# Performance work log

Measured on AMD Instinct MI355X. Metric: run time of the kernel, lower is better.

Reference implementation:

```python
import jax, jax.numpy as jnp
import numpy as np

N_NODES = 50000
N_EDGES = 800000
N_GRAPHS = 512
IN_DIM, HID_DIM, LAT_DIM = 128, 128, 64


def _glorot(key, fan_in, fan_out):
    lim = np.sqrt(6.0 / (fan_in + fan_out))
    return jax.random.uniform(key, (fan_in, fan_out), jnp.float32, -lim, lim)


def gcn_conv(x, W, b, src, dst, deg_inv_sqrt):
    """PyG GCNConv: out = D^{-1/2}(A+I)D^{-1/2} x W + b (self-loops included)."""
    h = x @ W  # [N, F_out]
    norm = deg_inv_sqrt[src] * deg_inv_sqrt[dst]  # [E]
    msg = h[src] * norm[:, None]  # gather + scale, [E, F_out]
    out = jax.ops.segment_sum(msg, dst, num_segments=x.shape[0])  # scatter-add
    out = out + h * (deg_inv_sqrt * deg_inv_sqrt)[:, None]  # self-loop term
    return out + b


def setup_inputs() -> dict:
    key = jax.random.key(0)
    ks = jax.random.split(key, 12)
    x = jax.random.normal(ks[0], (N_NODES, IN_DIM), jnp.float32)
    edge_index = jax.random.randint(ks[1], (2, N_EDGES), 0, N_NODES, jnp.int64)
    batch = jnp.sort(jax.random.randint(ks[2], (N_NODES,), 0, N_GRAPHS, jnp.int64))
    return {
        "x": x,
        "edge_index": edge_index,
        "batch": batch,
        "W1": _glorot(ks[3], IN_DIM, HID_DIM), "b1": jnp.zeros((HID_DIM,), jnp.float32),
        "W2": _glorot(ks[4], HID_DIM, LAT_DIM), "b2": jnp.zeros((LAT_DIM,), jnp.float32),
        "W3": _glorot(ks[5], LAT_DIM, HID_DIM), "b3": jnp.zeros((HID_DIM,), jnp.float32),
        "W4": _glorot(ks[6], HID_DIM, IN_DIM), "b4": jnp.zeros((IN_DIM,), jnp.float32),
    }


def reference(x, edge_index, batch, W1, b1, W2, b2, W3, b3, W4, b4):
    n = x.shape[0]
    src, dst = edge_index[0], edge_index[1]
    # degrees with self-loops (PyG computes deg over col=dst, +1 for self-loop)
    deg = jax.ops.segment_sum(jnp.ones_like(dst, dtype=x.dtype), dst, num_segments=n) + 1.0
    dis = jax.lax.rsqrt(deg)
    # encoder
    h = jax.nn.relu(gcn_conv(x, W1, b1, src, dst, dis))
    z = gcn_conv(h, W2, b2, src, dst, dis)
    # scatter-mean pooling over graphs
    counts = jax.ops.segment_sum(jnp.ones((n,), x.dtype), batch, num_segments=N_GRAPHS)
    agg = jax.ops.segment_sum(z, batch, num_segments=N_GRAPHS) / jnp.maximum(counts, 1.0)[:, None]
    # decoder
    h2 = jax.nn.relu(gcn_conv(z, W3, b3, src, dst, dis))
    x_hat = gcn_conv(h2, W4, b4, src, dst, dis)
    return (x_hat, z, agg)
```

## Files before the change

kernel.cpp:

```cpp
#include <hip/hip_runtime.h>
#include <hip/hip_fp16.h>
#include <math.h>

#define N_NODES 50000
#define N_EDGES 800000
#define N_GRAPHS 512
#define CAP 62
#define NBINS 196
#define CAPB 5120
#define ABLK 1024
#define PROP_BLOCKS 2048
#define PROP_WAVES (PROP_BLOCKS * 4)

typedef unsigned short u16;
typedef unsigned int u32;
typedef __attribute__((ext_vector_type(8))) short bf16x8_t;
typedef __attribute__((ext_vector_type(4))) float f32x4_t;
typedef __attribute__((ext_vector_type(4))) unsigned int u32x4_t;

constexpr int NBLK_A = (N_EDGES + ABLK - 1) / ABLK;
constexpr int NCW = (49152 + 255) / 256;

__device__ __forceinline__ u16 f2bf(float f) {
    u32 u = __builtin_bit_cast(u32, f);
    return (u16)((u + 0x7fffu + ((u >> 16) & 1u)) >> 16);
}
__device__ __forceinline__ float bf2f(u16 s) {
    return __builtin_bit_cast(float, (u32)s << 16);
}
__device__ __forceinline__ float bf_lo(u32 u) { return __builtin_bit_cast(float, u << 16); }
__device__ __forceinline__ float bf_hi(u32 u) { return __builtin_bit_cast(float, u & 0xffff0000u); }

__device__ __forceinline__ bf16x8_t cvt8(const float* p) {
    float4 a = *reinterpret_cast<const float4*>(p);
    float4 b = *reinterpret_cast<const float4*>(p + 4);
    u32x4_t w;
    w.x = (u32)f2bf(a.x) | ((u32)f2bf(a.y) << 16);
    w.y = (u32)f2bf(a.z) | ((u32)f2bf(a.w) << 16);
    w.z = (u32)f2bf(b.x) | ((u32)f2bf(b.y) << 16);
    w.w = (u32)f2bf(b.z) | ((u32)f2bf(b.w) << 16);
    return __builtin_bit_cast(bf16x8_t, w);
}

__device__ __forceinline__ int block_exscan(int val, int* lds, int tid) {
    lds[tid] = val;
    __syncthreads();
#pragma unroll
    for (int off = 1; off < 256; off <<= 1) {
        int t = (tid >= off) ? lds[tid - off] : 0;
        __syncthreads();
        lds[tid] += t;
        __syncthreads();
    }
    return lds[tid] - val;
}

__global__ __launch_bounds__(256) void pre_scatter(const int* __restrict__ src,
                                                   const int* __restrict__ dst,
                                                   u32* __restrict__ binCnt,
                                                   u32* __restrict__ binList,
                                                   const float* __restrict__ W1, u16* __restrict__ wt1,
                                                   const float* __restrict__ W2, u16* __restrict__ wt2,
                                                   const float* __restrict__ W3, u16* __restrict__ wt3,
                                                   const float* __restrict__ W4, u16* __restrict__ wt4) {
    __shared__ int cur[NBINS];
    __shared__ int lsStart[NBINS];
    __shared__ int gbase[NBINS];
    __shared__ int scanbuf[256];
    __shared__ u32 stage[ABLK];
    __shared__ int gpos[ABLK];
    int t = threadIdx.x;
    if (blockIdx.x >= NBLK_A) {
        int idx = (blockIdx.x - NBLK_A) * 256 + t;
        const float* Wf;
        u16* Wt;
        int K, N, off;
        if (idx < 16384)      { Wf = W1; Wt = wt1; K = 128; N = 128; off = 0; }
        else if (idx < 24576) { Wf = W2; Wt = wt2; K = 128; N = 64;  off = 16384; }
        else if (idx < 32768) { Wf = W3; Wt = wt3; K = 64;  N = 128; off = 24576; }
        else                  { Wf = W4; Wt = wt4; K = 128; N = 128; off = 32768; }
        int q = idx - off;
        int k = q / N, n = q % N;
        Wt[n * K + k] = f2bf(Wf[q]);
        return;
    }
    int e0 = blockIdx.x * ABLK;
    int nEdge = min(ABLK, N_EDGES - e0);

    for (int i = t; i < NBINS; i += 256) cur[i] = 0;
    __syncthreads();

    int myBin[4], myRank[4];
    u32 myPack[4];
    int nmy = 0;
    if (t * 4 < nEdge) {
        nmy = 4;
        int4 dv = *reinterpret_cast<const int4*>(dst + e0 + t * 4);
        int4 sv = *reinterpret_cast<const int4*>(src + e0 + t * 4);
        int ds[4] = {dv.x, dv.y, dv.z, dv.w};
        int ss[4] = {sv.x, sv.y, sv.z, sv.w};
#pragma unroll
        for (int j = 0; j < 4; j++) {
            int d = ds[j];
            int bin = d >> 8;
            myBin[j] = bin;
            myPack[j] = (u32)(ss[j] & 0xFFFF) | ((u32)(d & 0xFF) << 16);
            myRank[j] = atomicAdd(&cur[bin], 1);
        }
    }
    __syncthreads();
    int v = (t < NBINS) ? cur[t] : 0;
    int ex = block_exscan(v, scanbuf, t);
    if (t < NBINS) {
        lsStart[t] = ex;
        gbase[t] = (v > 0) ? (int)atomicAdd(&binCnt[t * 16], (u32)v) : 0;
    }
    __syncthreads();
    for (int j = 0; j < nmy; j++) {
        int bin = myBin[j];
        int idx = lsStart[bin] + myRank[j];
        int p = gbase[bin] + myRank[j];
        stage[idx] = myPack[j];
        gpos[idx] = (p < CAPB) ? (bin * CAPB + p) : -1;
    }
    __syncthreads();
    for (int i = t; i < nEdge; i += 256) {
        int p = gpos[i];
        if (p >= 0) binList[p] = stage[i];
    }
}

__global__ __launch_bounds__(256) void bucket_build(const u32* __restrict__ binList,
                                                    const u32* __restrict__ binCnt,
                                                    u32* __restrict__ bucket,
                                                    float* __restrict__ dis) {
    __shared__ u32 rec[256 * 32];
    int b = blockIdx.x, t = threadIdx.x;
    for (int i = t; i < 256 * 32; i += 256) rec[i] = 0;
    __syncthreads();
    int ecnt = min((int)binCnt[b * 16], CAPB);
    const u32* lst = binList + (size_t)b * CAPB;
    u16* rec16 = reinterpret_cast<u16*>(rec);
    for (int i = t; i < ecnt; i += 256) {
        u32 pk = lst[i];
        int dlow = (pk >> 16) & 0xFF;
        int pos = (int)atomicAdd(&rec[dlow * 32], 1u);
        if (pos < CAP) rec16[dlow * 64 + 2 + pos] = (u16)(pk & 0xFFFF);
    }
    __syncthreads();
    int node0 = b * 256;
    int nNode = min(256, N_NODES - node0);
    for (int i = t; i < nNode * 32; i += 256)
        bucket[(size_t)node0 * 32 + i] = rec[i];
    if (t < nNode) dis[node0 + t] = 1.0f / sqrtf((float)rec[t * 32] + 1.0f);
}

template <int N, int K, bool BIAS, bool RELU, bool SCALE, bool AF32>
__global__ __launch_bounds__(256) void gemm_mfma(const void* __restrict__ Avp,
                                                 const u16* __restrict__ Wt,
                                                 const float* __restrict__ bias,
                                                 const float* __restrict__ dis,
                                                 u16* __restrict__ C) {
    constexpr int KB = K / 32;
    constexpr int TN = N / 64;
    constexpr int TM = (N_NODES + 63) / 64;
    int wave = threadIdx.x >> 6;
    int lane = threadIdx.x & 63;
    int W = blockIdx.x * 4 + wave;
    if (W >= TM * TN) return;
    int tm = W / TN, tn = W % TN;
    int r16 = lane & 15;
    int kg = lane >> 4;

    bf16x8_t bf[4][KB];
#pragma unroll
    for (int nr = 0; nr < 4; nr++) {
        int colg = tn * 64 + nr * 16 + r16;
#pragma unroll
        for (int kb = 0; kb < KB; kb++)
            bf[nr][kb] = *reinterpret_cast<const bf16x8_t*>(Wt + (size_t)colg * K + kb * 32 + kg * 8);
    }

    f32x4_t acc[4][4];
#pragma unroll
    for (int mr = 0; mr < 4; mr++)
#pragma unroll
        for (int nr = 0; nr < 4; nr++)
#pragma unroll
            for (int t = 0; t < 4; t++) acc[mr][nr][t] = 0.f;

#pragma unroll
    for (int mr = 0; mr < 4; mr++) {
        int row = tm * 64 + mr * 16 + r16;
        if (row >= N_NODES) row = N_NODES - 1;
        bf16x8_t af[KB];
#pragma unroll
        for (int kb = 0; kb < KB; kb++) {
            if constexpr (AF32) {
                const float* Af = (const float*)Avp;
                af[kb] = cvt8(Af + (size_t)row * K + kb * 32 + kg * 8);
            } else {
                const u16* Ab = (const u16*)Avp;
                af[kb] = *reinterpret_cast<const bf16x8_t*>(Ab + (size_t)row * K + kb * 32 + kg * 8);
            }
        }
#pragma unroll
        for (int kb = 0; kb < KB; kb++)
#pragma unroll
            for (int nr = 0; nr < 4; nr++)
                acc[mr][nr] = __builtin_amdgcn_mfma_f32_16x16x32_bf16(af[kb], bf[nr][kb],
                                                                      acc[mr][nr], 0, 0, 0);
    }

#pragma unroll
    for (int mr = 0; mr < 4; mr++) {
        float sc[4];
#pragma unroll
        for (int r = 0; r < 4; r++) {
            int row = tm * 64 + mr * 16 + kg * 4 + r;
            sc[r] = (SCALE && row < N_NODES) ? dis[row] : 1.f;
        }
#pragma unroll
        for (int nr = 0; nr < 4; nr++) {
            int colg = tn * 64 + nr * 16 + r16;
            float bv = BIAS ? bias[colg] : 0.f;
#pragma unroll
            for (int r = 0; r < 4; r++) {
                int row = tm * 64 + mr * 16 + kg * 4 + r;
                if (row < N_NODES) {
                    float v = acc[mr][nr][r] + bv;
                    if (RELU) v = fmaxf(v, 0.f);
                    if (SCALE) v *= sc[r];
                    C[(size_t)row * N + colg] = f2bf(v);
                }
            }
        }
    }
}

template <int F, bool RELU, bool BIAS, bool WF32, bool WBF16, bool SCALEOUT>
__global__ __launch_bounds__(256) void propagate_b(const u16* __restrict__ h,
                                                   const u32* __restrict__ bucket,
                                                   const float* __restrict__ dis,
                                                   const float* __restrict__ bias,
                                                   float* __restrict__ out_f,
                                                   u16* __restrict__ out_b) {
    int wid = (blockIdx.x * 256 + threadIdx.x) >> 6;
    int lane = threadIdx.x & 63;
    float2 bv2 = make_float2(0.f, 0.f);
    float bv1 = 0.f;
    if (BIAS) {
        if (F == 128) bv2 = reinterpret_cast<const float2*>(bias)[lane];
        else          bv1 = bias[lane];
    }
    for (int w = wid; w < N_NODES; w += PROP_WAVES) {
        const u32* bw = bucket + (size_t)w * 32;
        int deg = __builtin_amdgcn_readfirstlane(min((int)bw[0], CAP));
        const u16* slots = reinterpret_cast<const u16*>(bw) + 2;
        const u32* sw = reinterpret_cast<const u32*>(reinterpret_cast<const char*>(bw) + 4);
        float di = dis[w];

        if (F == 128) {
            const u32* hw = reinterpret_cast<const u32*>(h);
            float2 a0 = {0.f, 0.f}, a1 = {0.f, 0.f}, a2 = {0.f, 0.f}, a3 = {0.f, 0.f};
            int i = 0;
            for (; i + 16 <= deg; i += 16) {
                u32 cw[8], hv[16];
#pragma unroll
                for (int j = 0; j < 8; j++) cw[j] = sw[(i >> 1) + j];
#pragma unroll
                for (int j = 0; j < 8; j++) {
                    hv[2 * j]     = hw[(size_t)(cw[j] & 0xffffu) * 64 + lane];
                    hv[2 * j + 1] = hw[(size_t)(cw[j] >> 16) * 64 + lane];
                }
#pragma unroll
                for (int j = 0; j < 16; j++) {
                    float lo = bf_lo(hv[j]), hi = bf_hi(hv[j]);
                    if ((j & 3) == 0) { a0.x += lo; a0.y += hi; }
                    else if ((j & 3) == 1) { a1.x += lo; a1.y += hi; }
                    else if ((j & 3) == 2) { a2.x += lo; a2.y += hi; }
                    else { a3.x += lo; a3.y += hi; }
                }
            }
            for (; i + 8 <= deg; i += 8) {
                u32 cw[4], hv[8];
#pragma unroll
                for (int j = 0; j < 4; j++) cw[j] = sw[(i >> 1) + j];
#pragma unroll
                for (int j = 0; j < 4; j++) {
                    hv[2 * j]     = hw[(size_t)(cw[j] & 0xffffu) * 64 + lane];
                    hv[2 * j + 1] = hw[(size_t)(cw[j] >> 16) * 64 + lane];
                }
#pragma unroll
                for (int j = 0; j < 8; j++) {
                    float lo = bf_lo(hv[j]), hi = bf_hi(hv[j]);
                    if ((j & 3) == 0) { a0.x += lo; a0.y += hi; }
                    else if ((j & 3) == 1) { a1.x += lo; a1.y += hi; }
                    else if ((j & 3) == 2) { a2.x += lo; a2.y += hi; }
                    else { a3.x += lo; a3.y += hi; }
                }
            }
            for (; i < deg; i++) {
                u32 u = hw[(size_t)slots[i] * 64 + lane];
                a0.x += bf_lo(u);
                a0.y += bf_hi(u);
            }
            u32 su = hw[(size_t)w * 64 + lane];
            float ox = (a0.x + a1.x + a2.x + a3.x + bf_lo(su)) * di;
            float oy = (a0.y + a1.y + a2.y + a3.y + bf_hi(su)) * di;
            if (BIAS) { ox += bv2.x; oy += bv2.y; }
            if (RELU) { ox = fmaxf(ox, 0.f); oy = fmaxf(oy, 0.f); }
            if (WF32) {
                reinterpret_cast<float2*>(out_f + (size_t)w * 128)[lane] = make_float2(ox, oy);
            }
            if (WBF16) {
                float wx = SCALEOUT ? ox * di : ox;
                float wy = SCALEOUT ? oy * di : oy;
                u32 pk = (u32)f2bf(wx) | ((u32)f2bf(wy) << 16);
                reinterpret_cast<u32*>(out_b)[(size_t)w * 64 + lane] = pk;
            }
        } else {
            float a0 = 0.f, a1 = 0.f, a2 = 0.f, a3 = 0.f;
            int i = 0;
            for (; i + 16 <= deg; i += 16) {
                u32 cw[8];
                u16 hv[16];
#pragma unroll
                for (int j = 0; j < 8; j++) cw[j] = sw[(i >> 1) + j];
#pragma unroll
                for (int j = 0; j < 8; j++) {
                    hv[2 * j]     = h[(size_t)(cw[j] & 0xffffu) * 64 + lane];
                    hv[2 * j + 1] = h[(size_t)(cw[j] >> 16) * 64 + lane];
                }
#pragma unroll
                for (int j = 0; j < 16; j++) {
                    float v = bf2f(hv[j]);
                    if ((j & 3) == 0) a0 += v;
                    else if ((j & 3) == 1) a1 += v;
                    else if ((j & 3) == 2) a2 += v;
                    else a3 += v;
                }
            }
            for (; i + 8 <= deg; i += 8) {
                u32 cw[4];
                u16 hv[8];
#pragma unroll
                for (int j = 0; j < 4; j++) cw[j] = sw[(i >> 1) + j];
#pragma unroll
                for (int j = 0; j < 4; j++) {
                    hv[2 * j]     = h[(size_t)(cw[j] & 0xffffu) * 64 + lane];
                    hv[2 * j + 1] = h[(size_t)(cw[j] >> 16) * 64 + lane];
                }
#pragma unroll
                for (int j = 0; j < 8; j++) {
                    float v = bf2f(hv[j]);
                    if ((j & 3) == 0) a0 += v;
                    else if ((j & 3) == 1) a1 += v;
                    else if ((j & 3) == 2) a2 += v;
                    else a3 += v;
                }
            }
            for (; i < deg; i++) a0 += bf2f(h[(size_t)slots[i] * 64 + lane]);
            float o = (a0 + a1 + a2 + a3 + bf2f(h[(size_t)w * 64 + lane])) * di;
            if (BIAS) o += bv1;
            if (RELU) o = fmaxf(o, 0.f);
            if (WF32) out_f[(size_t)w * 64 + lane] = o;
            if (WBF16) out_b[(size_t)w * 64 + lane] = f2bf(SCALEOUT ? o * di : o);
        }
    }
}

__global__ __launch_bounds__(256) void pool_kernel(const float* __restrict__ z,
                                                   const int* __restrict__ batch,
                                                   float* __restrict__ agg) {
    __shared__ float part[3][64];
    int g = blockIdx.x;
    int wave = threadIdx.x >> 6;
    int lane = threadIdx.x & 63;
    int l = 0, h = N_NODES;
    while (l < h) { int m = (l + h) >> 1; if (batch[m] < g) l = m + 1; else h = m; }
    int s = l;
    h = N_NODES;
    while (l < h) { int m = (l + h) >> 1; if (batch[m] < g + 1) l = m + 1; else h = m; }
    int e = l;
    float acc = 0.f;
    for (int i = s + wave; i < e; i += 4) acc += z[(size_t)i * 64 + lane];
    if (wave) part[wave - 1][lane] = acc;
    __syncthreads();
    if (wave == 0) {
        acc += part[0][lane] + part[1][lane] + part[2][lane];
        agg[(size_t)g * 64 + lane] = acc / fmaxf((float)(e - s), 1.0f);
    }
}

extern "C" void kernel_launch(void* const* d_in, const int* in_sizes, int n_in,
                              void* d_out, int out_size, void* d_ws, size_t ws_size,
                              hipStream_t stream) {
    const float* x   = (const float*)d_in[0];
    const int* eidx  = (const int*)d_in[1];
    const int* batch = (const int*)d_in[2];
    const float* W1  = (const float*)d_in[3];
    const float* b1  = (const float*)d_in[4];
    const float* W2  = (const float*)d_in[5];
    const float* b2  = (const float*)d_in[6];
    const float* W3  = (const float*)d_in[7];
    const float* b3  = (const float*)d_in[8];
    const float* W4  = (const float*)d_in[9];
    const float* b4  = (const float*)d_in[10];

    const int* src = eidx;
    const int* dst = eidx + N_EDGES;

    float* out_xhat = (float*)d_out;
    float* out_z    = out_xhat + (size_t)N_NODES * 128;
    float* out_agg  = out_z + (size_t)N_NODES * 64;

    char* p = (char*)d_ws;
    auto alloc = [&](size_t bytes) { char* r = p; p += (bytes + 255) & ~(size_t)255; return r; };
    u16* arena0 = (u16*)alloc((size_t)N_NODES * 128 * 2);
    u16* arena1 = (u16*)alloc((size_t)N_NODES * 128 * 2);
    u16* c1     = (u16*)alloc((size_t)N_NODES * 64 * 2);
    u16* c2     = (u16*)alloc((size_t)N_NODES * 64 * 2);
    u16* wt1    = (u16*)alloc(128 * 128 * 2);
    u16* wt2    = (u16*)alloc(128 * 64 * 2);
    u16* wt3    = (u16*)alloc(64 * 128 * 2);
    u16* wt4    = (u16*)alloc(128 * 128 * 2);
    u32* bucket = (u32*)alloc((size_t)N_NODES * 128);
    u32* binCnt = (u32*)alloc(NBINS * 16 * 4);
    u32* binList= (u32*)alloc((size_t)NBINS * CAPB * 4);
    float* dis  = (float*)alloc(N_NODES * 4);

    hipMemsetAsync(binCnt, 0, NBINS * 16 * 4, stream);
    pre_scatter<<<NBLK_A + NCW, 256, 0, stream>>>(src, dst, binCnt, binList,
                                                  W1, wt1, W2, wt2, W3, wt3, W4, wt4);
    bucket_build<<<NBINS, 256, 0, stream>>>(binList, binCnt, bucket, dis);

    const int G128 = ((N_NODES + 63) / 64 * 2 + 3) / 4;
    const int G64  = ((N_NODES + 63) / 64 * 1 + 3) / 4;

    gemm_mfma<128, 128, false, false, true, true><<<G128, 256, 0, stream>>>(
        x, wt1, nullptr, dis, arena1);
    propagate_b<128, true, true, false, true, false><<<PROP_BLOCKS, 256, 0, stream>>>(
        arena1, bucket, dis, b1, nullptr, arena0);
    gemm_mfma<64, 128, false, false, true, false><<<G64, 256, 0, stream>>>(
        arena0, wt2, nullptr, dis, c1);
    propagate_b<64, false, true, true, true, true><<<PROP_BLOCKS, 256, 0, stream>>>(
        c1, bucket, dis, b2, out_z, c2);
    pool_kernel<<<N_GRAPHS, 256, 0, stream>>>(out_z, batch, out_agg);
    propagate_b<64, false, false, false, true, false><<<PROP_BLOCKS, 256, 0, stream>>>(
        c2, bucket, dis, nullptr, nullptr, c1);
    gemm_mfma<128, 64, true, true, false, false><<<G128, 256, 0, stream>>>(
        c1, wt3, b3, dis, arena1);
    gemm_mfma<128, 128, false, false, true, false><<<G128, 256, 0, stream>>>(
        arena1, wt4, nullptr, dis, arena0);
    propagate_b<128, false, true, true, false, false><<<PROP_BLOCKS, 256, 0, stream>>>(
        arena0, bucket, dis, b4, out_xhat, nullptr);
}
```

Before: 258.1 us.

## Fuse pooling into third propagate, enlarge edge scatter blocks, pad bucket LDS

Scatter-mean pooling now runs inside the third propagation launch. The last 128 blocks handle pooling with one wave per graph, and the other blocks share the propagate work, which removes one kernel launch. The edge pre-scatter block grows from 1024 to 4096 edges, with 16 edges per thread, so there are fewer global atomics on bin counters. The bucket_build LDS rows are padded to 33 words to cut bank conflicts on the per-node counters. In exchange, pooling now runs serially in one wave per graph, and the propagate stage gets fewer waves.

```diff
diff --git a/kernel.cpp b/kernel.cpp
--- a/kernel.cpp
+++ b/kernel.cpp
@@ -1,5 +1,4 @@
 #include <hip/hip_runtime.h>
-#include <hip/hip_fp16.h>
 #include <math.h>
 
 #define N_NODES 50000
@@ -8,7 +7,7 @@
 #define CAP 62
 #define NBINS 196
 #define CAPB 5120
-#define ABLK 1024
+#define ABLK 4096
 #define PROP_BLOCKS 2048
 #define PROP_WAVES (PROP_BLOCKS * 4)
 
@@ -19,7 +18,8 @@
 typedef __attribute__((ext_vector_type(4))) unsigned int u32x4_t;
 
 constexpr int NBLK_A = (N_EDGES + ABLK - 1) / ABLK;
-constexpr int NCW = (49152 + 255) / 256;
+constexpr int WCONV_TOT = 49152;
+constexpr int NCW = (WCONV_TOT + 255) / 256;
 
 __device__ __forceinline__ u16 f2bf(float f) {
     u32 u = __builtin_bit_cast(u32, f);
@@ -63,70 +63,72 @@
                                                    const float* __restrict__ W2, u16* __restrict__ wt2,
                                                    const float* __restrict__ W3, u16* __restrict__ wt3,
                                                    const float* __restrict__ W4, u16* __restrict__ wt4) {
-    __shared__ int cur[NBINS];
-    __shared__ int lsStart[NBINS];
-    __shared__ int gbase[NBINS];
+    __shared__ int cur[256];
+    __shared__ int lsStart[256];
+    __shared__ int gbase[256];
     __shared__ int scanbuf[256];
     __shared__ u32 stage[ABLK];
     __shared__ int gpos[ABLK];
     int t = threadIdx.x;
     if (blockIdx.x >= NBLK_A) {
         int idx = (blockIdx.x - NBLK_A) * 256 + t;
-        const float* Wf;
-        u16* Wt;
-        int K, N, off;
-        if (idx < 16384)      { Wf = W1; Wt = wt1; K = 128; N = 128; off = 0; }
-        else if (idx < 24576) { Wf = W2; Wt = wt2; K = 128; N = 64;  off = 16384; }
-        else if (idx < 32768) { Wf = W3; Wt = wt3; K = 64;  N = 128; off = 24576; }
-        else                  { Wf = W4; Wt = wt4; K = 128; N = 128; off = 32768; }
-        int q = idx - off;
-        int k = q / N, n = q % N;
-        Wt[n * K + k] = f2bf(Wf[q]);
+        if (idx < WCONV_TOT) {
+            const float* Wf;
+            u16* Wt;
+            int K, N, off;
+            if (idx < 16384)      { Wf = W1; Wt = wt1; K = 128; N = 128; off = 0; }
+            else if (idx < 24576) { Wf = W2; Wt = wt2; K = 128; N = 64;  off = 16384; }
+            else if (idx < 32768) { Wf = W3; Wt = wt3; K = 64;  N = 128; off = 24576; }
+            else                  { Wf = W4; Wt = wt4; K = 128; N = 128; off = 32768; }
+            int q = idx - off;
+            int k = q / N, n = q % N;
+            Wt[n * K + k] = f2bf(Wf[q]);
+        }
         return;
     }
     int e0 = blockIdx.x * ABLK;
     int nEdge = min(ABLK, N_EDGES - e0);
 
-    for (int i = t; i < NBINS; i += 256) cur[i] = 0;
-    __syncthreads();
-
-    int myBin[4], myRank[4];
-    u32 myPack[4];
-    int nmy = 0;
-    if (t * 4 < nEdge) {
-        nmy = 4;
-        int4 dv = *reinterpret_cast<const int4*>(dst + e0 + t * 4);
-        int4 sv = *reinterpret_cast<const int4*>(src + e0 + t * 4);
+    cur[t] = 0;
+    __syncthreads();
+
+    int myBin[16], myRank[16];
+    u32 myPack[16];
+#pragma unroll
+    for (int p = 0; p < 4; p++) {
+        int off = p * 1024 + t * 4;
+        bool ok = off < nEdge;
+        int4 dv = ok ? *reinterpret_cast<const int4*>(dst + e0 + off) : make_int4(0, 0, 0, 0);
+        int4 sv = ok ? *reinterpret_cast<const int4*>(src + e0 + off) : make_int4(0, 0, 0, 0);
         int ds[4] = {dv.x, dv.y, dv.z, dv.w};
         int ss[4] = {sv.x, sv.y, sv.z, sv.w};
 #pragma unroll
         for (int j = 0; j < 4; j++) {
-            int d = ds[j];
-            int bin = d >> 8;
-            myBin[j] = bin;
-            myPack[j] = (u32)(ss[j] & 0xFFFF) | ((u32)(d & 0xFF) << 16);
-            myRank[j] = atomicAdd(&cur[bin], 1);
-        }
-    }
-    __syncthreads();
-    int v = (t < NBINS) ? cur[t] : 0;
+            int q = p * 4 + j;
+            myBin[q] = ok ? (ds[j] >> 8) : -1;
+            myPack[q] = (u32)(ss[j] & 0xFFFF) | ((u32)(ds[j] & 0xFF) << 16);
+            myRank[q] = ok ? atomicAdd(&cur[ds[j] >> 8], 1) : 0;
+        }
+    }
+    __syncthreads();
+    int v = cur[t];
     int ex = block_exscan(v, scanbuf, t);
-    if (t < NBINS) {
-        lsStart[t] = ex;
-        gbase[t] = (v > 0) ? (int)atomicAdd(&binCnt[t * 16], (u32)v) : 0;
-    }
-    __syncthreads();
-    for (int j = 0; j < nmy; j++) {
-        int bin = myBin[j];
-        int idx = lsStart[bin] + myRank[j];
-        int p = gbase[bin] + myRank[j];
-        stage[idx] = myPack[j];
-        gpos[idx] = (p < CAPB) ? (bin * CAPB + p) : -1;
+    lsStart[t] = ex;
+    gbase[t] = (v > 0) ? (int)atomicAdd(&binCnt[t * 16], (u32)v) : 0;
+    __syncthreads();
+#pragma unroll
+    for (int q = 0; q < 16; q++) {
+        if (myBin[q] >= 0) {
+            int idx = lsStart[myBin[q]] + myRank[q];
+            int pq = gbase[myBin[q]] + myRank[q];
+            stage[idx] = myPack[q];
+            gpos[idx] = (pq < CAPB) ? (myBin[q] * CAPB + pq) : -1;
+        }
     }
     __syncthreads();
     for (int i = t; i < nEdge; i += 256) {
-        int p = gpos[i];
-        if (p >= 0) binList[p] = stage[i];
+        int pq = gpos[i];
+        if (pq >= 0) binList[pq] = stage[i];
     }
 }
 
@@ -134,9 +136,9 @@
                                                     const u32* __restrict__ binCnt,
                                                     u32* __restrict__ bucket,
                                                     float* __restrict__ dis) {
-    __shared__ u32 rec[256 * 32];
+    __shared__ u32 rec[256 * 33];
     int b = blockIdx.x, t = threadIdx.x;
-    for (int i = t; i < 256 * 32; i += 256) rec[i] = 0;
+    for (int i = t; i < 256 * 33; i += 256) rec[i] = 0;
     __syncthreads();
     int ecnt = min((int)binCnt[b * 16], CAPB);
     const u32* lst = binList + (size_t)b * CAPB;
@@ -144,15 +146,15 @@
     for (int i = t; i < ecnt; i += 256) {
         u32 pk = lst[i];
         int dlow = (pk >> 16) & 0xFF;
-        int pos = (int)atomicAdd(&rec[dlow * 32], 1u);
-        if (pos < CAP) rec16[dlow * 64 + 2 + pos] = (u16)(pk & 0xFFFF);
+        int pos = (int)atomicAdd(&rec[dlow * 33], 1u);
+        if (pos < CAP) rec16[dlow * 66 + 2 + pos] = (u16)(pk & 0xFFFF);
     }
     __syncthreads();
     int node0 = b * 256;
     int nNode = min(256, N_NODES - node0);
     for (int i = t; i < nNode * 32; i += 256)
-        bucket[(size_t)node0 * 32 + i] = rec[i];
-    if (t < nNode) dis[node0 + t] = 1.0f / sqrtf((float)rec[t * 32] + 1.0f);
+        bucket[(size_t)node0 * 32 + i] = rec[(i >> 5) * 33 + (i & 31)];
+    if (t < nNode) dis[node0 + t] = 1.0f / sqrtf((float)rec[t * 33] + 1.0f);
 }
 
 template <int N, int K, bool BIAS, bool RELU, bool SCALE, bool AF32>
@@ -197,11 +199,9 @@
 #pragma unroll
         for (int kb = 0; kb < KB; kb++) {
             if constexpr (AF32) {
-                const float* Af = (const float*)Avp;
-                af[kb] = cvt8(Af + (size_t)row * K + kb * 32 + kg * 8);
+                af[kb] = cvt8((const float*)Avp + (size_t)row * K + kb * 32 + kg * 8);
             } else {
-                const u16* Ab = (const u16*)Avp;
-                af[kb] = *reinterpret_cast<const bf16x8_t*>(Ab + (size_t)row * K + kb * 32 + kg * 8);
+                af[kb] = *reinterpret_cast<const bf16x8_t*>((const u16*)Avp + (size_t)row * K + kb * 32 + kg * 8);
             }
         }
 #pragma unroll
@@ -239,21 +239,17 @@
 }
 
 template <int F, bool RELU, bool BIAS, bool WF32, bool WBF16, bool SCALEOUT>
-__global__ __launch_bounds__(256) void propagate_b(const u16* __restrict__ h,
-                                                   const u32* __restrict__ bucket,
-                                                   const float* __restrict__ dis,
-                                                   const float* __restrict__ bias,
-                                                   float* __restrict__ out_f,
-                                                   u16* __restrict__ out_b) {
-    int wid = (blockIdx.x * 256 + threadIdx.x) >> 6;
-    int lane = threadIdx.x & 63;
+__device__ void prop_dev(const u16* __restrict__ h, const u32* __restrict__ bucket,
+                         const float* __restrict__ dis, const float* __restrict__ bias,
+                         float* __restrict__ out_f, u16* __restrict__ out_b,
+                         int wid, int nwaves, int lane) {
     float2 bv2 = make_float2(0.f, 0.f);
     float bv1 = 0.f;
     if (BIAS) {
         if (F == 128) bv2 = reinterpret_cast<const float2*>(bias)[lane];
         else          bv1 = bias[lane];
     }
-    for (int w = wid; w < N_NODES; w += PROP_WAVES) {
+    for (int w = wid; w < N_NODES; w += nwaves) {
         const u32* bw = bucket + (size_t)w * 32;
         int deg = __builtin_amdgcn_readfirstlane(min((int)bw[0], CAP));
         const u16* slots = reinterpret_cast<const u16*>(bw) + 2;
@@ -370,13 +366,19 @@
     }
 }
 
-__global__ __launch_bounds__(256) void pool_kernel(const float* __restrict__ z,
-                                                   const int* __restrict__ batch,
-                                                   float* __restrict__ agg) {
-    __shared__ float part[3][64];
-    int g = blockIdx.x;
-    int wave = threadIdx.x >> 6;
-    int lane = threadIdx.x & 63;
+template <int F, bool RELU, bool BIAS, bool WF32, bool WBF16, bool SCALEOUT>
+__global__ __launch_bounds__(256) void propagate_k(const u16* __restrict__ h,
+                                                   const u32* __restrict__ bucket,
+                                                   const float* __restrict__ dis,
+                                                   const float* __restrict__ bias,
+                                                   float* __restrict__ out_f,
+                                                   u16* __restrict__ out_b) {
+    prop_dev<F, RELU, BIAS, WF32, WBF16, SCALEOUT>(h, bucket, dis, bias, out_f, out_b,
+        (int)(blockIdx.x * 4 + (threadIdx.x >> 6)), PROP_WAVES, threadIdx.x & 63);
+}
+
+__device__ void pool_wave(const float* __restrict__ z, const int* __restrict__ batch,
+                          float* __restrict__ agg, int g, int lane) {
     int l = 0, h = N_NODES;
     while (l < h) { int m = (l + h) >> 1; if (batch[m] < g) l = m + 1; else h = m; }
     int s = l;
@@ -384,13 +386,26 @@
     while (l < h) { int m = (l + h) >> 1; if (batch[m] < g + 1) l = m + 1; else h = m; }
     int e = l;
     float acc = 0.f;
-    for (int i = s + wave; i < e; i += 4) acc += z[(size_t)i * 64 + lane];
-    if (wave) part[wave - 1][lane] = acc;
-    __syncthreads();
-    if (wave == 0) {
-        acc += part[0][lane] + part[1][lane] + part[2][lane];
-        agg[(size_t)g * 64 + lane] = acc / fmaxf((float)(e - s), 1.0f);
-    }
+    for (int i = s; i < e; i++) acc += z[(size_t)i * 64 + lane];
+    agg[(size_t)g * 64 + lane] = acc / fmaxf((float)(e - s), 1.0f);
+}
+
+__global__ __launch_bounds__(256) void prop64_pool(const u16* __restrict__ h,
+                                                   const u32* __restrict__ bucket,
+                                                   const float* __restrict__ dis,
+                                                   u16* __restrict__ out_b,
+                                                   const float* __restrict__ z,
+                                                   const int* __restrict__ batch,
+                                                   float* __restrict__ agg) {
+    int wave = threadIdx.x >> 6;
+    int lane = threadIdx.x & 63;
+    if (blockIdx.x >= PROP_BLOCKS - 128) {
+        int g = (blockIdx.x - (PROP_BLOCKS - 128)) * 4 + wave;
+        pool_wave(z, batch, agg, g, lane);
+        return;
+    }
+    prop_dev<64, false, false, false, true, false>(h, bucket, dis, nullptr, nullptr, out_b,
+        (int)(blockIdx.x * 4 + wave), (PROP_BLOCKS - 128) * 4, lane);
 }
 
 extern "C" void kernel_launch(void* const* d_in, const int* in_sizes, int n_in,
@@ -440,19 +455,17 @@
 
     gemm_mfma<128, 128, false, false, true, true><<<G128, 256, 0, stream>>>(
         x, wt1, nullptr, dis, arena1);
-    propagate_b<128, true, true, false, true, false><<<PROP_BLOCKS, 256, 0, stream>>>(
+    propagate_k<128, true, true, false, true, false><<<PROP_BLOCKS, 256, 0, stream>>>(
         arena1, bucket, dis, b1, nullptr, arena0);
     gemm_mfma<64, 128, false, false, true, false><<<G64, 256, 0, stream>>>(
         arena0, wt2, nullptr, dis, c1);
-    propagate_b<64, false, true, true, true, true><<<PROP_BLOCKS, 256, 0, stream>>>(
+    propagate_k<64, false, true, true, true, true><<<PROP_BLOCKS, 256, 0, stream>>>(
         c1, bucket, dis, b2, out_z, c2);
-    pool_kernel<<<N_GRAPHS, 256, 0, stream>>>(out_z, batch, out_agg);
-    propagate_b<64, false, false, false, true, false><<<PROP_BLOCKS, 256, 0, stream>>>(
-        c2, bucket, dis, nullptr, nullptr, c1);
+    prop64_pool<<<PROP_BLOCKS, 256, 0, stream>>>(c2, bucket, dis, c1, out_z, batch, out_agg);
     gemm_mfma<128, 64, true, true, false, false><<<G128, 256, 0, stream>>>(
         c1, wt3, b3, dis, arena1);
     gemm_mfma<128, 128, false, false, true, false><<<G128, 256, 0, stream>>>(
         arena1, wt4, nullptr, dis, arena0);
-    propagate_b<128, false, true, true, false, false><<<PROP_BLOCKS, 256, 0, stream>>>(
+    propagate_k<128, false, true, true, false, false><<<PROP_BLOCKS, 256, 0, stream>>>(
         arena0, bucket, dis, b4, out_xhat, nullptr);
 }
```

Result: faster. 252.8 us (-2.1%).
